# Optimization experiments

Measured on AMD Instinct MI355X. Metric: run time of the kernel, lower is better.

The kernel has to match this reference:

```python
import jax, jax.numpy as jnp
import numpy as np

N_QUBITS = 4
Q_LAYERS = 3
BATCH = 16384


def setup_inputs() -> dict:
    key = jax.random.key(0)
    ks = jax.random.split(key, 12)

    def n(k, shape, s=0.1):
        return (s * jax.random.normal(k, shape)).astype(jnp.float32)

    return {
        "x": jax.random.normal(ks[0], (BATCH, 1, 28, 28), jnp.float32),
        "conv1_w": n(ks[1], (6, 1, 5, 5)),
        "conv1_b": n(ks[2], (6,)),
        "conv2_w": n(ks[3], (16, 6, 5, 5)),
        "conv2_b": n(ks[4], (16,)),
        "fc1_w": n(ks[5], (120, 256)),
        "fc1_b": n(ks[6], (120,)),
        "fc2_w": n(ks[7], (N_QUBITS, 120)),
        "fc2_b": n(ks[8], (N_QUBITS,)),
        "q_weights": n(ks[9], (Q_LAYERS, 1, N_QUBITS, 3), 0.01),
        "clf_w": n(ks[10], (10, N_QUBITS)),
        "clf_b": n(ks[11], (10,)),
    }


def _apply_1q(state, U, w):
    # state: (B, 2,2,2,2); U: (2,2) shared or (B,2,2) per-sample
    s = jnp.moveaxis(state, 1 + w, -1)
    if U.ndim == 2:
        s = jnp.einsum('ij,...j->...i', U, s)
    else:
        s = jnp.einsum('bij,b...j->b...i', U, s)
    return jnp.moveaxis(s, -1, 1 + w)


def _cnot(state, c, t):
    s = jnp.moveaxis(state, (1 + c, 1 + t), (-2, -1))
    s = jnp.concatenate([s[..., 0:1, :], s[..., 1:2, ::-1]], axis=-2)
    return jnp.moveaxis(s, (-2, -1), (1 + c, 1 + t))


def _rot(phi, theta, omega):
    # PennyLane Rot = RZ(omega) @ RY(theta) @ RZ(phi)
    c = jnp.cos(theta / 2)
    s = jnp.sin(theta / 2)
    m00 = jnp.exp(-0.5j * (phi + omega)) * c
    m01 = -jnp.exp(0.5j * (phi - omega)) * s
    m10 = jnp.exp(0.5j * (omega - phi)) * s
    m11 = jnp.exp(0.5j * (phi + omega)) * c
    return jnp.stack([jnp.stack([m00, m01]), jnp.stack([m10, m11])])


def _rx(a):
    # a: (B,) -> (B,2,2) RX matrices
    c = jnp.cos(a / 2) + 0j
    z = -1j * jnp.sin(a / 2)
    return jnp.stack([jnp.stack([c, z], -1), jnp.stack([z, c], -1)], -2)


def _circuit(angles, qw):
    # Data-reuploading circuit: per block, StronglyEntanglingLayers(1 sublayer, r=1)
    # then AngleEmbedding (RX). Returns <Z_i> per qubit, shape (B, 4).
    Bn = angles.shape[0]
    state = jnp.zeros((Bn, 16), jnp.complex64).at[:, 0].set(1.0)
    state = state.reshape(Bn, 2, 2, 2, 2)
    n_layers = qw.shape[0]
    for l in range(n_layers):
        for w in range(N_QUBITS):
            state = _apply_1q(state, _rot(qw[l, 0, w, 0], qw[l, 0, w, 1], qw[l, 0, w, 2]), w)
        for w in range(N_QUBITS):
            state = _cnot(state, w, (w + 1) % N_QUBITS)
        for w in range(N_QUBITS):
            state = _apply_1q(state, _rx(angles[:, w]), w)
    probs = jnp.abs(state) ** 2
    z = []
    for w in range(N_QUBITS):
        p = jnp.moveaxis(probs, 1 + w, -1).reshape(Bn, -1, 2)
        z.append(p[..., 0].sum(-1) - p[..., 1].sum(-1))
    return jnp.stack(z, axis=1).astype(jnp.float32)


def _conv(x, w, b):
    y = jax.lax.conv_general_dilated(x, w, (1, 1), 'VALID',
                                     dimension_numbers=('NCHW', 'OIHW', 'NCHW'))
    return y + b[None, :, None, None]


def _pool(x):
    return jax.lax.reduce_window(x, -jnp.inf, jax.lax.max,
                                 (1, 1, 2, 2), (1, 1, 2, 2), 'VALID')


def reference(x, conv1_w, conv1_b, conv2_w, conv2_b, fc1_w, fc1_b,
              fc2_w, fc2_b, q_weights, clf_w, clf_b):
    h = _pool(jax.nn.relu(_conv(x, conv1_w, conv1_b)))       # (B,6,12,12)
    h = _pool(jax.nn.relu(_conv(h, conv2_w, conv2_b)))       # (B,16,4,4)
    h = h.reshape(h.shape[0], -1)                            # (B,256)
    h = jax.nn.relu(h @ fc1_w.T + fc1_b)                     # (B,120)
    feat = h @ fc2_w.T + fc2_b                               # (B,4)
    angles = jnp.pi * jax.nn.sigmoid(feat)
    q_out = _circuit(angles, q_weights)                      # (B,4)
    logits = q_out @ clf_w.T + clf_b                         # (B,10)
    return logits
```

## Files before the change

### kernel.cpp

```cpp
#include <hip/hip_runtime.h>
#include <math.h>

#define BATCH_N 16384

typedef _Float16 half8 __attribute__((ext_vector_type(8)));
typedef float f32x4 __attribute__((ext_vector_type(4)));

#define C1W_F  0
#define BS1_F  200
#define BS2_F  208
#define FC2W_F 224
#define ROTM_F 708
#define RXCS_F 804
#define CWB_F  868
#define W2B_F  920
#define H2_F   2776
#define HS_F   3800
#define PW_F   4312
#define LDS_FLOATS 9304

__global__ __launch_bounds__(256, 4) void fused_model(
    const float* __restrict__ xg,
    const float* __restrict__ c1w, const float* __restrict__ c1b,
    const float* __restrict__ c2w, const float* __restrict__ c2b,
    const float* __restrict__ f1w, const float* __restrict__ f1b,
    const float* __restrict__ f2w, const float* __restrict__ f2b,
    const float* __restrict__ qw,  const float* __restrict__ cw,
    const float* __restrict__ cbias, float* __restrict__ out) {
    __shared__ float L[LDS_FLOATS];
    const int tid = threadIdx.x;
    const int b0 = blockIdx.x * 8;
    const int lane = tid & 63, wvi = tid >> 6;
    const int ml = lane & 15, q = lane >> 4;

    _Float16* W2BH = (_Float16*)(L + W2B_F);
    _Float16* H2H  = (_Float16*)(L + H2_F);
    _Float16* HSH  = (_Float16*)(L + HS_F);
    _Float16* H1CH = (_Float16*)(L + PW_F) + wvi * 2496;

    if (tid < 150) L[C1W_F + (tid % 25) * 8 + tid / 25] = c1w[tid];
    if (tid < 6)  L[BS1_F + tid] = c1b[tid];
    if (tid < 16) L[BS2_F + tid] = c2b[tid];
    for (int i = tid; i < 480; i += 256) L[FC2W_F + i] = f2w[i];
    if (tid < 4) L[FC2W_F + 480 + tid] = f2b[tid];
    if (tid < 40) L[CWB_F + tid] = cw[tid];
    if (tid < 10) L[CWB_F + 40 + tid] = cbias[tid];
    if (tid < 12) {
        const float phi = qw[tid * 3 + 0];
        const float th  = qw[tid * 3 + 1];
        const float om  = qw[tid * 3 + 2];
        const float ct = cosf(0.5f * th), st = sinf(0.5f * th);
        const float ap = 0.5f * (phi + om), bm = 0.5f * (phi - om);
        const float ca = cosf(ap), sa = sinf(ap);
        const float cbm = cosf(bm), sbm = sinf(bm);
        float* R = &L[ROTM_F + tid * 8];
        R[0] =  ct * ca;  R[1] = -ct * sa;
        R[2] = -st * cbm; R[3] = -st * sbm;
        R[4] =  st * cbm; R[5] = -st * sbm;
        R[6] =  ct * ca;  R[7] =  ct * sa;
    }
    for (int i = tid; i < 3712; i += 256) {
        const int oc = i / 232, r = i - oc * 232;
        float v = 0.f;
        if (r < 200) {
            const int pix = r >> 3, ic = r & 7;
            if (ic < 6) v = c2w[oc * 150 + ic * 25 + pix];
        }
        W2BH[oc * 232 + r] = (_Float16)v;
    }
    __syncthreads();

    for (int t = lane; t < 288; t += 64) {
        const int s = t >= 144 ? 1 : 0;
        const int r = t - s * 144;
        const int py = r / 12, px = r - (r / 12) * 12;
        const float* xp = xg + (size_t)(b0 + 2 * wvi + s) * 784 + (2 * py) * 28 + 2 * px;

        float p[6][6];
#pragma unroll
        for (int rr = 0; rr < 6; rr++) {
            const float2 a = *(const float2*)(xp + rr * 28);
            const float2 b = *(const float2*)(xp + rr * 28 + 2);
            const float2 c = *(const float2*)(xp + rr * 28 + 4);
            p[rr][0] = a.x; p[rr][1] = a.y; p[rr][2] = b.x;
            p[rr][3] = b.y; p[rr][4] = c.x; p[rr][5] = c.y;
        }

        float acc[6][4];
#pragma unroll
        for (int o = 0; o < 6; o++) {
            const float bv = L[BS1_F + o];
            acc[o][0] = bv; acc[o][1] = bv; acc[o][2] = bv; acc[o][3] = bv;
        }
#pragma unroll
        for (int ky = 0; ky < 5; ky++)
#pragma unroll
            for (int kx = 0; kx < 5; kx++) {
                const int k = ky * 5 + kx;
                const float4 wA = *(const float4*)&L[C1W_F + k * 8];
                const float2 wB = *(const float2*)&L[C1W_F + k * 8 + 4];
                const float p00 = p[ky][kx],     p01 = p[ky][kx + 1];
                const float p10 = p[ky + 1][kx], p11 = p[ky + 1][kx + 1];
                acc[0][0] = fmaf(wA.x, p00, acc[0][0]); acc[0][1] = fmaf(wA.x, p01, acc[0][1]);
                acc[0][2] = fmaf(wA.x, p10, acc[0][2]); acc[0][3] = fmaf(wA.x, p11, acc[0][3]);
                acc[1][0] = fmaf(wA.y, p00, acc[1][0]); acc[1][1] = fmaf(wA.y, p01, acc[1][1]);
                acc[1][2] = fmaf(wA.y, p10, acc[1][2]); acc[1][3] = fmaf(wA.y, p11, acc[1][3]);
                acc[2][0] = fmaf(wA.z, p00, acc[2][0]); acc[2][1] = fmaf(wA.z, p01, acc[2][1]);
                acc[2][2] = fmaf(wA.z, p10, acc[2][2]); acc[2][3] = fmaf(wA.z, p11, acc[2][3]);
                acc[3][0] = fmaf(wA.w, p00, acc[3][0]); acc[3][1] = fmaf(wA.w, p01, acc[3][1]);
                acc[3][2] = fmaf(wA.w, p10, acc[3][2]); acc[3][3] = fmaf(wA.w, p11, acc[3][3]);
                acc[4][0] = fmaf(wB.x, p00, acc[4][0]); acc[4][1] = fmaf(wB.x, p01, acc[4][1]);
                acc[4][2] = fmaf(wB.x, p10, acc[4][2]); acc[4][3] = fmaf(wB.x, p11, acc[4][3]);
                acc[5][0] = fmaf(wB.y, p00, acc[5][0]); acc[5][1] = fmaf(wB.y, p01, acc[5][1]);
                acc[5][2] = fmaf(wB.y, p10, acc[5][2]); acc[5][3] = fmaf(wB.y, p11, acc[5][3]);
            }

        union { _Float16 h[8]; uint4 u; } O;
#pragma unroll
        for (int o = 0; o < 6; o++) {
            const float m = fmaxf(fmaxf(acc[o][0], acc[o][1]), fmaxf(acc[o][2], acc[o][3]));
            O.h[o] = (_Float16)fmaxf(m, 0.f);
        }
        O.h[6] = (_Float16)0.f; O.h[7] = (_Float16)0.f;
        *(uint4*)(H1CH + s * 1248 + (py * 13 + px) * 8) = O.u;
    }
    __builtin_amdgcn_wave_barrier();

    {
        f32x4 c2a[2][4];
#pragma unroll
        for (int a = 0; a < 2; a++)
#pragma unroll
            for (int b = 0; b < 4; b++) c2a[a][b] = (f32x4){0.f, 0.f, 0.f, 0.f};

#pragma unroll
        for (int ks = 0; ks < 7; ks++) {
            const half8 bfrag = *(const half8*)(W2BH + ml * 232 + ks * 32 + q * 8);
            int tp = ks * 4 + q; if (tp > 24) tp = 24;
            const int poff = (tp / 5) * 13 + (tp % 5);
#pragma unroll
            for (int si = 0; si < 2; si++) {
                const _Float16* hp = H1CH + si * 1248;
#pragma unroll
                for (int t = 0; t < 4; t++) {
                    const int cp = t * 16 + ml;
                    const int unit = (cp >> 3) * 13 + (cp & 7) + poff;
                    const half8 afrag = *(const half8*)(hp + unit * 8);
                    c2a[si][t] = __builtin_amdgcn_mfma_f32_16x16x32_f16(afrag, bfrag, c2a[si][t], 0, 0, 0);
                }
            }
        }

        const float bv = L[BS2_F + ml];
#pragma unroll
        for (int si = 0; si < 2; si++) {
#pragma unroll
            for (int t = 0; t < 4; t++) {
                const float c0 = c2a[si][t][0] + bv, c1 = c2a[si][t][1] + bv;
                const float c2 = c2a[si][t][2] + bv, c3 = c2a[si][t][3] + bv;
                float px0 = fmaxf(c0, c1), px1 = fmaxf(c2, c3);
                px0 = fmaxf(px0, __shfl_xor(px0, 32));
                px1 = fmaxf(px1, __shfl_xor(px1, 32));
                if (lane < 32) {
                    union { _Float16 h[2]; unsigned u; } P2;
                    P2.h[0] = (_Float16)fmaxf(px0, 0.f);
                    P2.h[1] = (_Float16)fmaxf(px1, 0.f);
                    *(unsigned*)(H2H + (2 * wvi + si) * 256 + ml * 16 + t * 4 + (q & 1) * 2) = P2.u;
                }
            }
        }
    }
    __syncthreads();

    {
        f32x4 fcC[2];
        fcC[0] = (f32x4){0.f, 0.f, 0.f, 0.f};
        fcC[1] = (f32x4){0.f, 0.f, 0.f, 0.f};
        const int ms = (ml < 8) ? ml : 0;
#pragma unroll
        for (int ks = 0; ks < 8; ks++) {
            const half8 afrag = *(const half8*)(H2H + ms * 256 + ks * 32 + q * 8);
#pragma unroll
            for (int ti = 0; ti < 2; ti++) {
                const int n = (wvi + 4 * ti) * 16 + ml;
                half8 bfrag;
                if (n < 120) {
                    const float* wp = f1w + (size_t)n * 256 + ks * 32 + q * 8;
                    const float4 u = *(const float4*)wp;
                    const float4 v = *(const float4*)(wp + 4);
                    bfrag[0] = (_Float16)u.x; bfrag[1] = (_Float16)u.y;
                    bfrag[2] = (_Float16)u.z; bfrag[3] = (_Float16)u.w;
                    bfrag[4] = (_Float16)v.x; bfrag[5] = (_Float16)v.y;
                    bfrag[6] = (_Float16)v.z; bfrag[7] = (_Float16)v.w;
                } else {
#pragma unroll
                    for (int j = 0; j < 8; j++) bfrag[j] = (_Float16)0.f;
                }
                fcC[ti] = __builtin_amdgcn_mfma_f32_16x16x32_f16(afrag, bfrag, fcC[ti], 0, 0, 0);
            }
        }
        if (q < 2) {
#pragma unroll
            for (int ti = 0; ti < 2; ti++) {
                const int n = (wvi + 4 * ti) * 16 + ml;
                if (n < 120) {
                    const float bb = f1b[n];
#pragma unroll
                    for (int rg = 0; rg < 4; rg++) {
                        const int s = q * 4 + rg;
                        HSH[s * 128 + n] = (_Float16)fmaxf(fcC[ti][rg] + bb, 0.f);
                    }
                }
            }
        }
    }
    __syncthreads();

    if (tid < 32) {
        const int s = tid >> 2, m = tid & 3;
        float f = L[FC2W_F + 480 + m];
        for (int nn = 0; nn < 120; nn += 8) {
            const half8 hv = *(const half8*)(HSH + s * 128 + nn);
            const float* wp = &L[FC2W_F + m * 120 + nn];
            f = fmaf(wp[0], (float)hv[0], f); f = fmaf(wp[1], (float)hv[1], f);
            f = fmaf(wp[2], (float)hv[2], f); f = fmaf(wp[3], (float)hv[3], f);
            f = fmaf(wp[4], (float)hv[4], f); f = fmaf(wp[5], (float)hv[5], f);
            f = fmaf(wp[6], (float)hv[6], f); f = fmaf(wp[7], (float)hv[7], f);
        }
        const float ang = 3.14159265358979323846f / (1.f + expf(-f));
        L[RXCS_F + tid]      = cosf(0.5f * ang);
        L[RXCS_F + 32 + tid] = sinf(0.5f * ang);
    }
    __syncthreads();

    if (tid < 128) {
        const int s = tid >> 4, a = tid & 15;
        float ar = (a == 0) ? 1.f : 0.f, ai = 0.f;

#pragma unroll
        for (int l = 0; l < 3; l++) {
#pragma unroll
            for (int w = 0; w < 4; w++) {
                const float* R = &L[ROTM_F + (l * 4 + w) * 8];
                const int mask = 8 >> w;
                const float pr = __shfl_xor(ar, mask);
                const float pi = __shfl_xor(ai, mask);
                const bool bit = (a & mask) != 0;
                const float lr = bit ? pr : ar, li = bit ? pi : ai;
                const float hr = bit ? ar : pr, hi = bit ? ai : pi;
                const float Ar = bit ? R[4] : R[0], Ai = bit ? R[5] : R[1];
                const float Br = bit ? R[6] : R[2], Bi = bit ? R[7] : R[3];
                ar = Ar * lr - Ai * li + Br * hr - Bi * hi;
                ai = Ar * li + Ai * lr + Br * hi + Bi * hr;
            }
#pragma unroll
            for (int w = 0; w < 4; w++) {
                const int mc = 8 >> w, mt = 8 >> ((w + 1) & 3);
                const float pr = __shfl_xor(ar, mt);
                const float pi = __shfl_xor(ai, mt);
                const bool ctrl = (a & mc) != 0;
                ar = ctrl ? pr : ar;
                ai = ctrl ? pi : ai;
            }
#pragma unroll
            for (int w = 0; w < 4; w++) {
                const int mask = 8 >> w;
                const float c  = L[RXCS_F + s * 4 + w];
                const float s2 = L[RXCS_F + 32 + s * 4 + w];
                const float pr = __shfl_xor(ar, mask);
                const float pi = __shfl_xor(ai, mask);
                const float nr = fmaf(c, ar, s2 * pi);
                const float ni = fmaf(c, ai, -s2 * pr);
                ar = nr; ai = ni;
            }
        }

        float v = ar * ar + ai * ai;
#pragma unroll
        for (int d = 1; d < 16; d <<= 1) {
            const float pv = __shfl_xor(v, d);
            v = (a & d) ? (pv - v) : (v + pv);
        }

        if (a < 10) {
            const int base = (tid & 63) & ~15;
            float lg = L[CWB_F + 40 + a];
#pragma unroll
            for (int w = 0; w < 4; w++) {
                const float zw = __shfl(v, base | (8 >> w));
                lg = fmaf(L[CWB_F + a * 4 + w], zw, lg);
            }
            out[(size_t)(b0 + s) * 10 + a] = lg;
        }
    }
}

extern "C" void kernel_launch(void* const* d_in, const int* in_sizes, int n_in,
                              void* d_out, int out_size, void* d_ws, size_t ws_size,
                              hipStream_t stream) {
    const float* x   = (const float*)d_in[0];
    const float* c1w = (const float*)d_in[1];
    const float* c1b = (const float*)d_in[2];
    const float* c2w = (const float*)d_in[3];
    const float* c2b = (const float*)d_in[4];
    const float* f1w = (const float*)d_in[5];
    const float* f1b = (const float*)d_in[6];
    const float* f2w = (const float*)d_in[7];
    const float* f2b = (const float*)d_in[8];
    const float* qw  = (const float*)d_in[9];
    const float* cw  = (const float*)d_in[10];
    const float* cb  = (const float*)d_in[11];
    float* out = (float*)d_out;

    fused_model<<<BATCH_N / 8, 256, 0, stream>>>(x, c1w, c1b, c2w, c2b,
                                                 f1w, f1b, f2w, f2b,
                                                 qw, cw, cb, out);
}
```

Measured before the change: 181.6 us.

## Compute conv1 with packed fp16 dot2 and shrink LDS to raise occupancy

Conv1 now packs input pixels and weights into fp16 pairs and accumulates with v_dot2 into fp32, replacing the scalar fp32 FMA loop. This halves the instruction count for the first convolution. The conv2 output buffer and the staging area are aliased onto the per-wave conv1 scratch region to cut LDS use, and launch bounds are raised from 4 to 5 blocks per CU to improve occupancy. In exchange, conv1 inputs are rounded to fp16 with round-toward-zero conversion, which loses precision, and the buffer aliasing needs correct barrier ordering.

```diff
diff --git a/kernel.cpp b/kernel.cpp
--- a/kernel.cpp
+++ b/kernel.cpp
@@ -4,22 +4,21 @@
 #define BATCH_N 16384
 
 typedef _Float16 half8 __attribute__((ext_vector_type(8)));
+typedef __fp16 h2 __attribute__((ext_vector_type(2)));
 typedef float f32x4 __attribute__((ext_vector_type(4)));
 
-#define C1W_F  0
-#define BS1_F  200
-#define BS2_F  208
-#define FC2W_F 224
-#define ROTM_F 708
-#define RXCS_F 804
-#define CWB_F  868
-#define W2B_F  920
-#define H2_F   2776
-#define HS_F   3800
-#define PW_F   4312
-#define LDS_FLOATS 9304
-
-__global__ __launch_bounds__(256, 4) void fused_model(
+#define C1P_F  0
+#define BS1_F  120
+#define BS2_F  128
+#define FC2W_F 144
+#define ROTM_F 628
+#define RXCS_F 724
+#define CWB_F  788
+#define W2B_F  840
+#define PW_F   2696
+#define LDS_FLOATS 7688
+
+__global__ __launch_bounds__(256, 5) void fused_model(
     const float* __restrict__ xg,
     const float* __restrict__ c1w, const float* __restrict__ c1b,
     const float* __restrict__ c2w, const float* __restrict__ c2b,
@@ -34,11 +33,20 @@
     const int ml = lane & 15, q = lane >> 4;
 
     _Float16* W2BH = (_Float16*)(L + W2B_F);
-    _Float16* H2H  = (_Float16*)(L + H2_F);
-    _Float16* HSH  = (_Float16*)(L + HS_F);
-    _Float16* H1CH = (_Float16*)(L + PW_F) + wvi * 2496;
-
-    if (tid < 150) L[C1W_F + (tid % 25) * 8 + tid / 25] = c1w[tid];
+    _Float16* PWH  = (_Float16*)(L + PW_F);
+    _Float16* H1CH = PWH + wvi * 2496;
+    _Float16* HSH  = PWH + 512;
+
+    if (tid < 120) {
+        const int oc = tid / 20, r = tid - oc * 20, ky = r >> 2, j = r & 3;
+        const float* wb = c1w + oc * 25 + ky * 5;
+        float lo, hi;
+        if (j == 0)      { lo = wb[0]; hi = wb[1]; }
+        else if (j == 1) { lo = wb[2]; hi = wb[3]; }
+        else if (j == 2) { lo = wb[4]; hi = 0.f;   }
+        else             { lo = 0.f;   hi = wb[4]; }
+        ((h2*)&L[C1P_F])[tid] = __builtin_amdgcn_cvt_pkrtz(lo, hi);
+    }
     if (tid < 6)  L[BS1_F + tid] = c1b[tid];
     if (tid < 16) L[BS2_F + tid] = c2b[tid];
     for (int i = tid; i < 480; i += 256) L[FC2W_F + i] = f2w[i];
@@ -76,50 +84,45 @@
         const int py = r / 12, px = r - (r / 12) * 12;
         const float* xp = xg + (size_t)(b0 + 2 * wvi + s) * 784 + (2 * py) * 28 + 2 * px;
 
-        float p[6][6];
+        h2 A[6][3], S[6][2];
 #pragma unroll
         for (int rr = 0; rr < 6; rr++) {
             const float2 a = *(const float2*)(xp + rr * 28);
             const float2 b = *(const float2*)(xp + rr * 28 + 2);
             const float2 c = *(const float2*)(xp + rr * 28 + 4);
-            p[rr][0] = a.x; p[rr][1] = a.y; p[rr][2] = b.x;
-            p[rr][3] = b.y; p[rr][4] = c.x; p[rr][5] = c.y;
-        }
-
-        float acc[6][4];
-#pragma unroll
-        for (int o = 0; o < 6; o++) {
-            const float bv = L[BS1_F + o];
-            acc[o][0] = bv; acc[o][1] = bv; acc[o][2] = bv; acc[o][3] = bv;
-        }
-#pragma unroll
-        for (int ky = 0; ky < 5; ky++)
-#pragma unroll
-            for (int kx = 0; kx < 5; kx++) {
-                const int k = ky * 5 + kx;
-                const float4 wA = *(const float4*)&L[C1W_F + k * 8];
-                const float2 wB = *(const float2*)&L[C1W_F + k * 8 + 4];
-                const float p00 = p[ky][kx],     p01 = p[ky][kx + 1];
-                const float p10 = p[ky + 1][kx], p11 = p[ky + 1][kx + 1];
-                acc[0][0] = fmaf(wA.x, p00, acc[0][0]); acc[0][1] = fmaf(wA.x, p01, acc[0][1]);
-                acc[0][2] = fmaf(wA.x, p10, acc[0][2]); acc[0][3] = fmaf(wA.x, p11, acc[0][3]);
-                acc[1][0] = fmaf(wA.y, p00, acc[1][0]); acc[1][1] = fmaf(wA.y, p01, acc[1][1]);
-                acc[1][2] = fmaf(wA.y, p10, acc[1][2]); acc[1][3] = fmaf(wA.y, p11, acc[1][3]);
-                acc[2][0] = fmaf(wA.z, p00, acc[2][0]); acc[2][1] = fmaf(wA.z, p01, acc[2][1]);
-                acc[2][2] = fmaf(wA.z, p10, acc[2][2]); acc[2][3] = fmaf(wA.z, p11, acc[2][3]);
-                acc[3][0] = fmaf(wA.w, p00, acc[3][0]); acc[3][1] = fmaf(wA.w, p01, acc[3][1]);
-                acc[3][2] = fmaf(wA.w, p10, acc[3][2]); acc[3][3] = fmaf(wA.w, p11, acc[3][3]);
-                acc[4][0] = fmaf(wB.x, p00, acc[4][0]); acc[4][1] = fmaf(wB.x, p01, acc[4][1]);
-                acc[4][2] = fmaf(wB.x, p10, acc[4][2]); acc[4][3] = fmaf(wB.x, p11, acc[4][3]);
-                acc[5][0] = fmaf(wB.y, p00, acc[5][0]); acc[5][1] = fmaf(wB.y, p01, acc[5][1]);
-                acc[5][2] = fmaf(wB.y, p10, acc[5][2]); acc[5][3] = fmaf(wB.y, p11, acc[5][3]);
-            }
+            A[rr][0] = __builtin_amdgcn_cvt_pkrtz(a.x, a.y);
+            A[rr][1] = __builtin_amdgcn_cvt_pkrtz(b.x, b.y);
+            A[rr][2] = __builtin_amdgcn_cvt_pkrtz(c.x, c.y);
+            S[rr][0] = __builtin_amdgcn_cvt_pkrtz(a.y, b.x);
+            S[rr][1] = __builtin_amdgcn_cvt_pkrtz(b.y, c.x);
+        }
 
         union { _Float16 h[8]; uint4 u; } O;
 #pragma unroll
-        for (int o = 0; o < 6; o++) {
-            const float m = fmaxf(fmaxf(acc[o][0], acc[o][1]), fmaxf(acc[o][2], acc[o][3]));
-            O.h[o] = (_Float16)fmaxf(m, 0.f);
+        for (int oc = 0; oc < 6; oc++) {
+            union { uint4 v; h2 h[4]; } W[5];
+#pragma unroll
+            for (int ky = 0; ky < 5; ky++)
+                W[ky].v = ((const uint4*)&L[C1P_F])[oc * 5 + ky];
+            const float bv = L[BS1_F + oc];
+            float a00 = bv, a01 = bv, a10 = bv, a11 = bv;
+#pragma unroll
+            for (int ky = 0; ky < 5; ky++) {
+                a00 = __builtin_amdgcn_fdot2(A[ky][0],     W[ky].h[0], a00, false);
+                a00 = __builtin_amdgcn_fdot2(A[ky][1],     W[ky].h[1], a00, false);
+                a00 = __builtin_amdgcn_fdot2(A[ky][2],     W[ky].h[2], a00, false);
+                a01 = __builtin_amdgcn_fdot2(S[ky][0],     W[ky].h[0], a01, false);
+                a01 = __builtin_amdgcn_fdot2(S[ky][1],     W[ky].h[1], a01, false);
+                a01 = __builtin_amdgcn_fdot2(A[ky][2],     W[ky].h[3], a01, false);
+                a10 = __builtin_amdgcn_fdot2(A[ky + 1][0], W[ky].h[0], a10, false);
+                a10 = __builtin_amdgcn_fdot2(A[ky + 1][1], W[ky].h[1], a10, false);
+                a10 = __builtin_amdgcn_fdot2(A[ky + 1][2], W[ky].h[2], a10, false);
+                a11 = __builtin_amdgcn_fdot2(S[ky + 1][0], W[ky].h[0], a11, false);
+                a11 = __builtin_amdgcn_fdot2(S[ky + 1][1], W[ky].h[1], a11, false);
+                a11 = __builtin_amdgcn_fdot2(A[ky + 1][2], W[ky].h[3], a11, false);
+            }
+            const float m = fmaxf(fmaxf(a00, a01), fmaxf(a10, a11));
+            O.h[oc] = (_Float16)fmaxf(m, 0.f);
         }
         O.h[6] = (_Float16)0.f; O.h[7] = (_Float16)0.f;
         *(uint4*)(H1CH + s * 1248 + (py * 13 + px) * 8) = O.u;
@@ -165,7 +168,7 @@
                     union { _Float16 h[2]; unsigned u; } P2;
                     P2.h[0] = (_Float16)fmaxf(px0, 0.f);
                     P2.h[1] = (_Float16)fmaxf(px1, 0.f);
-                    *(unsigned*)(H2H + (2 * wvi + si) * 256 + ml * 16 + t * 4 + (q & 1) * 2) = P2.u;
+                    *(unsigned*)(PWH + wvi * 2496 + si * 256 + ml * 16 + t * 4 + (q & 1) * 2) = P2.u;
                 }
             }
         }
@@ -177,9 +180,10 @@
         fcC[0] = (f32x4){0.f, 0.f, 0.f, 0.f};
         fcC[1] = (f32x4){0.f, 0.f, 0.f, 0.f};
         const int ms = (ml < 8) ? ml : 0;
+        const _Float16* h2p = PWH + (ms >> 1) * 2496 + (ms & 1) * 256;
 #pragma unroll
         for (int ks = 0; ks < 8; ks++) {
-            const half8 afrag = *(const half8*)(H2H + ms * 256 + ks * 32 + q * 8);
+            const half8 afrag = *(const half8*)(h2p + ks * 32 + q * 8);
 #pragma unroll
             for (int ti = 0; ti < 2; ti++) {
                 const int n = (wvi + 4 * ti) * 16 + ml;
```

After: 182.5 us. Within noise of the previous version (+0.5%).
